# Performance work log

Measured on AMD Instinct MI355X. Metric: run time of the kernel, lower is better.

The kernel has to match this reference:

```python
import jax, jax.numpy as jnp
import numpy as np

N = 50000
E = 1600000
F = 128
G = 64  # number of graphs in the batch


def gat_layer(x, src, dst, W, a_src, a_dst, bias, heads, out_dim, concat):
    n = x.shape[0]
    h = (x @ W).reshape(n, heads, out_dim)                      # [N,H,D]
    alpha_src = jnp.sum(h * a_src, axis=-1)                     # [N,H]
    alpha_dst = jnp.sum(h * a_dst, axis=-1)                     # [N,H]
    e = jax.nn.leaky_relu(alpha_src[src] + alpha_dst[dst], negative_slope=0.2)  # [E,H]
    # segment softmax over edges grouped by destination node
    m = jax.ops.segment_max(e, dst, num_segments=n)
    m = jnp.where(jnp.isfinite(m), m, 0.0)
    ex = jnp.exp(e - m[dst])
    denom = jax.ops.segment_sum(ex, dst, num_segments=n)
    alpha = ex / (denom[dst] + 1e-16)                           # [E,H]
    msg = h[src] * alpha[:, :, None]                            # [E,H,D]
    out = jax.ops.segment_sum(msg, dst, num_segments=n)         # [N,H,D]
    if concat:
        out = out.reshape(n, heads * out_dim)
    else:
        out = out.mean(axis=1)
    return out + bias


def setup_inputs() -> dict:
    key = jax.random.key(0)
    ks = jax.random.split(key, 12)
    x = jax.random.normal(ks[0], (N, F), dtype=jnp.float32)
    edge_index = jax.random.randint(ks[1], (2, E), 0, N, dtype=jnp.int32)
    batch = jnp.sort(jax.random.randint(ks[2], (N,), 0, G, dtype=jnp.int32))
    s = 0.1
    W1 = jax.random.normal(ks[3], (F, 4 * 32), dtype=jnp.float32) * s
    a_src1 = jax.random.normal(ks[4], (4, 32), dtype=jnp.float32) * s
    a_dst1 = jax.random.normal(ks[5], (4, 32), dtype=jnp.float32) * s
    b1 = jnp.zeros((4 * 32,), dtype=jnp.float32)
    W2 = jax.random.normal(ks[6], (4 * 32, 2 * 16), dtype=jnp.float32) * s
    a_src2 = jax.random.normal(ks[7], (2, 16), dtype=jnp.float32) * s
    a_dst2 = jax.random.normal(ks[8], (2, 16), dtype=jnp.float32) * s
    b2 = jnp.zeros((16,), dtype=jnp.float32)
    fcW = jax.random.normal(ks[9], (16, 1), dtype=jnp.float32) * s
    fcb = jnp.zeros((1,), dtype=jnp.float32)
    return {"x": x, "edge_index": edge_index, "batch": batch,
            "W1": W1, "a_src1": a_src1, "a_dst1": a_dst1, "b1": b1,
            "W2": W2, "a_src2": a_src2, "a_dst2": a_dst2, "b2": b2,
            "fcW": fcW, "fcb": fcb}


def reference(x, edge_index, batch, W1, a_src1, a_dst1, b1, W2, a_src2, a_dst2, b2, fcW, fcb):
    n = x.shape[0]
    # PyG GATConv default: add self loops
    loops = jnp.arange(n, dtype=edge_index.dtype)
    src = jnp.concatenate([edge_index[0], loops])
    dst = jnp.concatenate([edge_index[1], loops])
    # eval mode: dropouts are no-ops
    h = jax.nn.relu(gat_layer(x, src, dst, W1, a_src1, a_dst1, b1, 4, 32, True))
    h = gat_layer(h, src, dst, W2, a_src2, a_dst2, b2, 2, 16, False)
    # global mean pool over graphs
    sums = jax.ops.segment_sum(h, batch, num_segments=G)        # [G,16]
    counts = jax.ops.segment_sum(jnp.ones((n,), h.dtype), batch, num_segments=G)
    pooled = sums / jnp.maximum(counts, 1.0)[:, None]
    return pooled @ fcW + fcb                                   # [G,1]
```

## Files before the change

kernel.cpp:

```cpp
#include <hip/hip_runtime.h>

#define LRELU(x) ((x) > 0.f ? (x) : 0.2f*(x))
typedef unsigned int uint;

__device__ inline unsigned short f2bf(float f) {
    union { float f; unsigned u; } v; v.f = f;
    unsigned r = v.u + 0x7FFF + ((v.u >> 16) & 1);
    return (unsigned short)(r >> 16);
}
__device__ inline uint packbf(float a, float b) {
    return (uint)f2bf(a) | ((uint)f2bf(b) << 16);
}
__device__ inline float bflo(uint u){ union{uint u; float f;}v; v.u = u<<16; return v.f; }
__device__ inline float bfhi(uint u){ union{uint u; float f;}v; v.u = u & 0xFFFF0000u; return v.f; }
__device__ inline float f4get(const float4& v, int i) {
    return i==0 ? v.x : i==1 ? v.y : i==2 ? v.z : v.w;
}


#define CSR_SHIFT 7
#define CSR_NBLK  512

__global__ __launch_bounds__(256) void bucket_count_kernel(
    const int* __restrict__ dst, int E, int chunk, int nb,
    int* __restrict__ blockCntT)
{
    __shared__ int cnt[1024];
    int t = threadIdx.x, k = blockIdx.x;
    for (int i = t; i < nb; i += 256) cnt[i] = 0;
    __syncthreads();
    int e0 = k * chunk, e1 = min(e0 + chunk, E);
    for (int e = e0 + t; e < e1; e += 256)
        atomicAdd(&cnt[dst[e] >> CSR_SHIFT], 1);
    __syncthreads();
    for (int b = t; b < nb; b += 256)
        blockCntT[b * CSR_NBLK + k] = cnt[b];
}

__global__ __launch_bounds__(512) void row_scan_kernel(
    int* __restrict__ blockCntT, int* __restrict__ tot)
{
    __shared__ int sm[512];
    int b = blockIdx.x, t = threadIdx.x;
    int* row = blockCntT + b * CSR_NBLK;
    int v = row[t];
    sm[t] = v;
    __syncthreads();
    for (int off = 1; off < 512; off <<= 1) {
        int u = (t >= off) ? sm[t - off] : 0;
        __syncthreads(); sm[t] += u; __syncthreads();
    }
    row[t] = sm[t] - v;
    if (t == 511) tot[b] = sm[511];
}

__global__ __launch_bounds__(1024) void total_scan_kernel(
    const int* __restrict__ tot, int nb, int* __restrict__ bucketBase)
{
    __shared__ int sm[1024];
    int t = threadIdx.x;
    int v = (t < nb) ? tot[t] : 0;
    sm[t] = v;
    __syncthreads();
    for (int off = 1; off < 1024; off <<= 1) {
        int u = (t >= off) ? sm[t - off] : 0;
        __syncthreads(); sm[t] += u; __syncthreads();
    }
    if (t < nb) bucketBase[t] = sm[t] - v;
    if (t == 1023) bucketBase[nb] = sm[1023];
}

__global__ __launch_bounds__(256) void bucket_scatter_kernel(
    const int* __restrict__ src, const int* __restrict__ dst, int E, int chunk, int nb,
    const int* __restrict__ blockCntT, const int* __restrict__ bucketBase,
    uint* __restrict__ ebuf)
{
    __shared__ int cur[1024];
    int t = threadIdx.x, k = blockIdx.x;
    for (int b = t; b < nb; b += 256)
        cur[b] = bucketBase[b] + blockCntT[b * CSR_NBLK + k];
    __syncthreads();
    int e0 = k * chunk, e1 = min(e0 + chunk, E);
    for (int e = e0 + t; e < e1; e += 256) {
        int d = dst[e], s_ = src[e];
        int pos = atomicAdd(&cur[d >> CSR_SHIFT], 1);
        ebuf[pos] = ((uint)s_ << 7) | (uint)(d & 127);
    }
}

__global__ __launch_bounds__(256) void local_csr_kernel(
    const uint* __restrict__ ebuf, const int* __restrict__ bucketBase,
    int n, int E, int* __restrict__ rowptr, int* __restrict__ csr)
{
    __shared__ int lbase[1 << CSR_SHIFT];
    __shared__ int lcur[1 << CSR_SHIFT];
    __shared__ int ldeg[1 << CSR_SHIFT];
    int b = blockIdx.x, t = threadIdx.x;
    int n0 = b << CSR_SHIFT;
    int base = bucketBase[b], end = bucketBase[b + 1];
    if (t < (1 << CSR_SHIFT)) ldeg[t] = 0;
    __syncthreads();
    for (int e = base + t; e < end; e += 256)
        atomicAdd(&ldeg[ebuf[e] & 127], 1);
    __syncthreads();
    if (t == 0) {
        int run = base;
        for (int i = 0; i < (1 << CSR_SHIFT); ++i) {
            lbase[i] = run; lcur[i] = run; run += ldeg[i];
        }
    }
    __syncthreads();
    int node = n0 + t;
    if (t < (1 << CSR_SHIFT) && node < n) rowptr[node] = lbase[t];
    if (b == 0 && t == 0) rowptr[n] = E;
    for (int e = base + t; e < end; e += 256) {
        uint ed = ebuf[e];
        int pos = atomicAdd(&lcur[ed & 127], 1);
        csr[pos] = (int)(ed >> 7);
    }
}


template<int COLS, int HEADS>
__global__ __launch_bounds__(256) void gemm_alpha_kernel(
    const float* __restrict__ x, const float* __restrict__ W,
    const float* __restrict__ a_src, const float* __restrict__ a_dst,
    uint* __restrict__ hq, float* __restrict__ as_out,
    float* __restrict__ ad_out, int n)
{
    constexpr int K = 128;
    constexpr int CPT = COLS / 8;
    constexpr int NPT = 4;
    constexpr int DIM = COLS / HEADS;
    constexpr int TPH = DIM / CPT;
    constexpr int NSLOT = COLS / 4;
    __shared__ float4 WL[K * NSLOT];

    int t = threadIdx.x;
    for (int idx = t * 4; idx < K * COLS; idx += 1024) {
        float4 w = *(const float4*)(W + idx);
        int k = idx / COLS, c = idx % COLS;
        int slot = c >> 2;
        if (COLS == 128) slot = (slot >> 2) | ((slot & 3) << 3);
        WL[k * NSLOT + slot] = w;
    }
    __syncthreads();

    int m_ = t & 7;
    int node0 = blockIdx.x * (32 * NPT) + (t >> 3) * NPT;
    if (node0 >= n) return;
    int c0 = m_ * CPT;

    const float* xr[NPT];
#pragma unroll
    for (int i = 0; i < NPT; i++) xr[i] = x + (size_t)min(node0 + i, n - 1) * K;

    float acc[NPT][CPT];
#pragma unroll
    for (int i = 0; i < NPT; i++)
#pragma unroll
        for (int q = 0; q < CPT; q++) acc[i][q] = 0.f;

    for (int k4 = 0; k4 < K; k4 += 4) {
        float4 xv[NPT];
#pragma unroll
        for (int i = 0; i < NPT; i++) xv[i] = *(const float4*)(xr[i] + k4);
#pragma unroll
        for (int kk = 0; kk < 4; kk++) {
#pragma unroll
            for (int j = 0; j < CPT / 4; j++) {
                int slot = (COLS == 128) ? (m_ | (j << 3)) : m_;
                float4 w = WL[(k4 + kk) * NSLOT + slot];
#pragma unroll
                for (int i = 0; i < NPT; i++) {
                    float xa = f4get(xv[i], kk);
                    acc[i][j*4+0] += xa * w.x;
                    acc[i][j*4+1] += xa * w.y;
                    acc[i][j*4+2] += xa * w.z;
                    acc[i][j*4+3] += xa * w.w;
                }
            }
        }
    }

    int head = c0 / DIM, lc = c0 - head * DIM;
    float asc[CPT], adc[CPT];
#pragma unroll
    for (int q = 0; q < CPT; q++) {
        asc[q] = a_src[head * DIM + lc + q];
        adc[q] = a_dst[head * DIM + lc + q];
    }

#pragma unroll
    for (int i = 0; i < NPT; i++) {
        int node = node0 + i;
        if (node >= n) break;
        if constexpr (COLS == 128) {
            uint wds[4];
#pragma unroll
            for (int j = 0; j < 4; j++) {
                int u = 0;
                u = __builtin_amdgcn_cvt_pk_fp8_f32(acc[i][j*4+0], acc[i][j*4+1], u, false);
                u = __builtin_amdgcn_cvt_pk_fp8_f32(acc[i][j*4+2], acc[i][j*4+3], u, true);
                wds[j] = (uint)u;
            }
            *(uint4*)(hq + (size_t)node * 32 + m_ * 4) = make_uint4(wds[0], wds[1], wds[2], wds[3]);
        } else {
            uint w0 = packbf(acc[i][0], acc[i][1]);
            uint w1 = packbf(acc[i][2], acc[i][3]);
            *(uint2*)(hq + (size_t)node * 16 + m_ * 2) = make_uint2(w0, w1);
        }
        float ps = 0.f, pd = 0.f;
#pragma unroll
        for (int q = 0; q < CPT; q++) {
            ps += acc[i][q] * asc[q];
            pd += acc[i][q] * adc[q];
        }
#pragma unroll
        for (int off = 1; off < TPH; off <<= 1) {
            ps += __shfl_xor(ps, off);
            pd += __shfl_xor(pd, off);
        }
        if ((m_ & (TPH - 1)) == 0) {
            as_out[node * HEADS + head] = ps;
            ad_out[node * HEADS + head] = pd;
        }
    }
}


__global__ __launch_bounds__(256) void agg1_kernel(
    const float* __restrict__ as1f, const float* __restrict__ ad1f,
    const uint* __restrict__ h1q, const int* __restrict__ rowptr,
    const int* __restrict__ csr, const float* __restrict__ b1,
    float* __restrict__ hout, int n)
{
    int t = threadIdx.x;
    int w = t >> 6, tw = t & 63;
    int g = tw >> 3, l = tw & 7;
    int head = l >> 1;
    int node = blockIdx.x * 4 + w;
    if (node >= n) return;

    float adh = ad1f[node * 4 + head];
    int rp = rowptr[node], re = rowptr[node + 1];

    float acc[16];
#pragma unroll
    for (int i = 0; i < 16; i++) acc[i] = 0.f;
    float den = 0.f;

#pragma unroll 2
    for (int e = rp + g; e < re; e += 8) {
        int s = csr[e];
        float a = as1f[s * 4 + head];
        uint4 u = *(const uint4*)(h1q + ((size_t)s << 5) + (l << 2));
        float ex = __expf(LRELU(a + adh));
        den += ex;
        uint ua[4] = {u.x, u.y, u.z, u.w};
#pragma unroll
        for (int j = 0; j < 4; j++) {
            auto p0 = __builtin_amdgcn_cvt_pk_f32_fp8(ua[j], false);
            auto p1 = __builtin_amdgcn_cvt_pk_f32_fp8(ua[j], true);
            acc[j*4+0] += ex * p0[0]; acc[j*4+1] += ex * p0[1];
            acc[j*4+2] += ex * p1[0]; acc[j*4+3] += ex * p1[1];
        }
    }

    if (g == 0) {
        float a = as1f[node * 4 + head];
        float ex = __expf(LRELU(a + adh));
        den += ex;
        uint4 u = *(const uint4*)(h1q + ((size_t)node << 5) + (l << 2));
        uint ua[4] = {u.x, u.y, u.z, u.w};
#pragma unroll
        for (int j = 0; j < 4; j++) {
            auto p0 = __builtin_amdgcn_cvt_pk_f32_fp8(ua[j], false);
            auto p1 = __builtin_amdgcn_cvt_pk_f32_fp8(ua[j], true);
            acc[j*4+0] += ex * p0[0]; acc[j*4+1] += ex * p0[1];
            acc[j*4+2] += ex * p1[0]; acc[j*4+3] += ex * p1[1];
        }
    }

#pragma unroll
    for (int i = 0; i < 16; i++) {
        acc[i] += __shfl_xor(acc[i], 8);
        acc[i] += __shfl_xor(acc[i], 16);
        acc[i] += __shfl_xor(acc[i], 32);
    }
    den += __shfl_xor(den, 8);
    den += __shfl_xor(den, 16);
    den += __shfl_xor(den, 32);

    if (g == 0) {
        float inv = 1.f / (den + 1e-16f);
        const float4* b4 = (const float4*)b1;
#pragma unroll
        for (int j = 0; j < 4; j++) {
            float4 bv = b4[(l << 2) + j];
            float4 o;
            o.x = fmaxf(acc[j*4+0] * inv + bv.x, 0.f);
            o.y = fmaxf(acc[j*4+1] * inv + bv.y, 0.f);
            o.z = fmaxf(acc[j*4+2] * inv + bv.z, 0.f);
            o.w = fmaxf(acc[j*4+3] * inv + bv.w, 0.f);
            ((float4*)hout)[(size_t)node * 32 + (l << 2) + j] = o;
        }
    }
}


__global__ __launch_bounds__(256) void agg2_kernel(
    const float* __restrict__ as2f, const float* __restrict__ ad2f,
    const uint* __restrict__ h2q, const int* __restrict__ rowptr,
    const int* __restrict__ csr, const float* __restrict__ b2,
    float* __restrict__ hf, int n)
{
    int t = threadIdx.x;
    int w = t >> 6, tw = t & 63;
    int g = tw >> 3, l = tw & 7;
    int head = l >> 2;
    int node = blockIdx.x * 4 + w;
    if (node >= n) return;

    float adh = ad2f[node * 2 + head];
    int rp = rowptr[node], re = rowptr[node + 1];

    float acc[4] = {0.f, 0.f, 0.f, 0.f};
    float den = 0.f;

#pragma unroll 2
    for (int e = rp + g; e < re; e += 8) {
        int s = csr[e];
        float a = as2f[s * 2 + head];
        uint2 u = *(const uint2*)(h2q + ((size_t)s << 4) + (l << 1));
        float ex = __expf(LRELU(a + adh));
        den += ex;
        acc[0] += ex * bflo(u.x); acc[1] += ex * bfhi(u.x);
        acc[2] += ex * bflo(u.y); acc[3] += ex * bfhi(u.y);
    }

    if (g == 0) {
        float a = as2f[node * 2 + head];
        float ex = __expf(LRELU(a + adh));
        den += ex;
        uint2 u = *(const uint2*)(h2q + ((size_t)node << 4) + (l << 1));
        acc[0] += ex * bflo(u.x); acc[1] += ex * bfhi(u.x);
        acc[2] += ex * bflo(u.y); acc[3] += ex * bfhi(u.y);
    }

#pragma unroll
    for (int i = 0; i < 4; i++) {
        acc[i] += __shfl_xor(acc[i], 8);
        acc[i] += __shfl_xor(acc[i], 16);
        acc[i] += __shfl_xor(acc[i], 32);
    }
    den += __shfl_xor(den, 8);
    den += __shfl_xor(den, 16);
    den += __shfl_xor(den, 32);

    float inv = 1.f / (den + 1e-16f);
    float v0 = acc[0] * inv, v1 = acc[1] * inv, v2 = acc[2] * inv, v3 = acc[3] * inv;
    float o0 = 0.5f * (v0 + __shfl_xor(v0, 4));
    float o1 = 0.5f * (v1 + __shfl_xor(v1, 4));
    float o2 = 0.5f * (v2 + __shfl_xor(v2, 4));
    float o3 = 0.5f * (v3 + __shfl_xor(v3, 4));
    if (g == 0 && l < 4) {
        float4 o;
        o.x = o0 + b2[4*l+0]; o.y = o1 + b2[4*l+1];
        o.z = o2 + b2[4*l+2]; o.w = o3 + b2[4*l+3];
        *(float4*)(hf + (size_t)node * 16 + 4 * l) = o;
    }
}


__global__ __launch_bounds__(256) void pool_kernel(
    const float* __restrict__ hf, const int* __restrict__ batch,
    float* __restrict__ sums, float* __restrict__ counts, int n)
{
    int t = threadIdx.x;
    int d = t & 15, j = t >> 4;
    int base = blockIdx.x * 256 + j * 16;
    float run = 0.f, cnt = 0.f;
    int cg = -1;
    for (int i = 0; i < 16; ++i) {
        int nn = base + i;
        if (nn >= n) break;
        int g = batch[nn];
        if (g != cg) {
            if (cg >= 0) { atomicAdd(&sums[cg * 16 + d], run); if (d == 0) atomicAdd(&counts[cg], cnt); }
            cg = g; run = 0.f; cnt = 0.f;
        }
        run += hf[(size_t)nn * 16 + d];
        cnt += 1.f;
    }
    if (cg >= 0) { atomicAdd(&sums[cg * 16 + d], run); if (d == 0) atomicAdd(&counts[cg], cnt); }
}

__global__ void final_kernel(const float* __restrict__ sums, const float* __restrict__ counts,
                             const float* __restrict__ fcW, const float* __restrict__ fcb,
                             float* __restrict__ out, int G)
{
    int g = blockIdx.x * 64 + threadIdx.x;
    if (g < G) {
        float c = fmaxf(counts[g], 1.f);
        float s = 0.f;
        for (int dd = 0; dd < 16; ++dd) s += (sums[g * 16 + dd] / c) * fcW[dd];
        out[g] = s + fcb[0];
    }
}


extern "C" void kernel_launch(void* const* d_in, const int* in_sizes, int n_in,
                              void* d_out, int out_size, void* d_ws, size_t ws_size,
                              hipStream_t stream)
{
    const float* x      = (const float*)d_in[0];
    const int*   ei     = (const int*)d_in[1];
    const int*   batch  = (const int*)d_in[2];
    const float* W1     = (const float*)d_in[3];
    const float* a_src1 = (const float*)d_in[4];
    const float* a_dst1 = (const float*)d_in[5];
    const float* b1     = (const float*)d_in[6];
    const float* W2     = (const float*)d_in[7];
    const float* a_src2 = (const float*)d_in[8];
    const float* a_dst2 = (const float*)d_in[9];
    const float* b2     = (const float*)d_in[10];
    const float* fcW    = (const float*)d_in[11];
    const float* fcb    = (const float*)d_in[12];
    float* out = (float*)d_out;

    int n = in_sizes[0] / 128;
    int E = in_sizes[1] / 2;
    int G = out_size;
    const int* srcA = ei;
    const int* dstA = ei + E;

    int nb = (n + (1 << CSR_SHIFT) - 1) >> CSR_SHIFT;
    int chunk = (E + CSR_NBLK - 1) / CSR_NBLK;

    char* p = (char*)d_ws;
    auto alloc = [&](size_t bytes) { char* r = p; p += (bytes + 255) & ~(size_t)255; return r; };
    int*   blockCntT  = (int*)alloc((size_t)nb * CSR_NBLK * 4);
    int*   tot        = (int*)alloc((size_t)nb * 4);
    int*   bucketBase = (int*)alloc((size_t)(nb + 1) * 4);
    int*   rowptr     = (int*)alloc((size_t)(n + 1) * 4);
    int*   csr        = (int*)alloc((size_t)E * 4);
    uint*  h1q        = (uint*)alloc((size_t)n * 32 * 4);
    float* as1        = (float*)alloc((size_t)n * 16);
    float* ad1        = (float*)alloc((size_t)n * 16);
    float* hrelu      = (float*)alloc((size_t)n * 128 * 4);
    uint*  h2q        = (uint*)alloc((size_t)n * 16 * 4);
    float* as2        = (float*)alloc((size_t)n * 8);
    float* ad2        = (float*)alloc((size_t)n * 8);
    float* hf         = (float*)alloc((size_t)n * 16 * 4);
    float* sums       = (float*)alloc((size_t)G * 16 * 4 + (size_t)G * 4);
    float* counts     = sums + G * 16;

    uint* ebuf = (uint*)hrelu;

    hipMemsetAsync(sums, 0, (size_t)G * 16 * 4 + (size_t)G * 4, stream);

    bucket_count_kernel<<<CSR_NBLK, 256, 0, stream>>>(dstA, E, chunk, nb, blockCntT);
    row_scan_kernel<<<nb, 512, 0, stream>>>(blockCntT, tot);
    total_scan_kernel<<<1, 1024, 0, stream>>>(tot, nb, bucketBase);
    bucket_scatter_kernel<<<CSR_NBLK, 256, 0, stream>>>(srcA, dstA, E, chunk, nb,
                                                        blockCntT, bucketBase, ebuf);
    local_csr_kernel<<<nb, 256, 0, stream>>>(ebuf, bucketBase, n, E, rowptr, csr);

    int gb = (n + 127) / 128;
    gemm_alpha_kernel<128, 4><<<gb, 256, 0, stream>>>(x, W1, a_src1, a_dst1, h1q, as1, ad1, n);
    agg1_kernel<<<(n + 3) / 4, 256, 0, stream>>>(as1, ad1, h1q, rowptr, csr, b1, hrelu, n);
    gemm_alpha_kernel<32, 2><<<gb, 256, 0, stream>>>(hrelu, W2, a_src2, a_dst2, h2q, as2, ad2, n);
    agg2_kernel<<<(n + 3) / 4, 256, 0, stream>>>(as2, ad2, h2q, rowptr, csr, b2, hf, n);
    pool_kernel<<<(n + 255) / 256, 256, 0, stream>>>(hf, batch, sums, counts, n);
    final_kernel<<<1, 64, 0, stream>>>(sums, counts, fcW, fcb, out, G);
}
```

Baseline: 195.9 us.

## Precompute per-edge attention exponentials in fp16 before aggregation kernels

Adds a destination array to the CSR build and two per-edge kernels that compute exp(leaky_relu(alpha_src+alpha_dst)) for all heads once, storing them as packed fp16 in CSR order. The aggregation kernels then read these values with a coalesced load instead of doing a random gather of alpha_src plus an exp per lane, and their inner-loop unroll grows from 2 to 4. This costs extra kernel launches, an extra E-sized dst array write, and per-edge exp buffers (8 bytes per edge for layer 1). Storing the exponentials in fp16 reduces precision and can overflow for large logits.

Result: slower. 244.3 us (+24.8%).

```diff
diff --git a/kernel.cpp b/kernel.cpp
--- a/kernel.cpp
+++ b/kernel.cpp
@@ -2,11 +2,12 @@
 
 #define LRELU(x) ((x) > 0.f ? (x) : 0.2f*(x))
 typedef unsigned int uint;
-
-__device__ inline unsigned short f2bf(float f) {
+typedef unsigned short ushort;
+
+__device__ inline ushort f2bf(float f) {
     union { float f; unsigned u; } v; v.f = f;
     unsigned r = v.u + 0x7FFF + ((v.u >> 16) & 1);
-    return (unsigned short)(r >> 16);
+    return (ushort)(r >> 16);
 }
 __device__ inline uint packbf(float a, float b) {
     return (uint)f2bf(a) | ((uint)f2bf(b) << 16);
@@ -16,6 +17,8 @@
 __device__ inline float f4get(const float4& v, int i) {
     return i==0 ? v.x : i==1 ? v.y : i==2 ? v.z : v.w;
 }
+__device__ inline ushort f2h(float f){ _Float16 h=(_Float16)f; union{_Float16 h; ushort u;}v; v.h=h; return v.u; }
+__device__ inline float h2f(ushort u){ union{ushort u; _Float16 h;}v; v.u=u; return (float)v.h; }
 
 
 #define CSR_SHIFT 7
@@ -90,7 +93,8 @@
 
 __global__ __launch_bounds__(256) void local_csr_kernel(
     const uint* __restrict__ ebuf, const int* __restrict__ bucketBase,
-    int n, int E, int* __restrict__ rowptr, int* __restrict__ csr)
+    int n, int E, int* __restrict__ rowptr, int* __restrict__ csr,
+    int* __restrict__ dstarr)
 {
     __shared__ int lbase[1 << CSR_SHIFT];
     __shared__ int lcur[1 << CSR_SHIFT];
@@ -115,9 +119,42 @@
     if (b == 0 && t == 0) rowptr[n] = E;
     for (int e = base + t; e < end; e += 256) {
         uint ed = ebuf[e];
-        int pos = atomicAdd(&lcur[ed & 127], 1);
+        int ld = (int)(ed & 127);
+        int pos = atomicAdd(&lcur[ld], 1);
         csr[pos] = (int)(ed >> 7);
-    }
+        dstarr[pos] = n0 + ld;
+    }
+}
+
+
+__global__ __launch_bounds__(256) void edge_ex1_kernel(
+    const float4* __restrict__ as1, const float4* __restrict__ ad1,
+    const int* __restrict__ csr, const int* __restrict__ dstarr,
+    ushort* __restrict__ exq, int E)
+{
+    int p = blockIdx.x * 256 + threadIdx.x;
+    if (p >= E) return;
+    int s = csr[p], d = dstarr[p];
+    float4 a = as1[s], b = ad1[d];
+    ushort4 o;
+    o.x = f2h(__expf(LRELU(a.x + b.x)));
+    o.y = f2h(__expf(LRELU(a.y + b.y)));
+    o.z = f2h(__expf(LRELU(a.z + b.z)));
+    o.w = f2h(__expf(LRELU(a.w + b.w)));
+    *(ushort4*)(exq + (size_t)p * 4) = o;
+}
+
+__global__ __launch_bounds__(256) void edge_ex2_kernel(
+    const float2* __restrict__ as2, const float2* __restrict__ ad2,
+    const int* __restrict__ csr, const int* __restrict__ dstarr,
+    uint* __restrict__ exq, int E)
+{
+    int p = blockIdx.x * 256 + threadIdx.x;
+    if (p >= E) return;
+    int s = csr[p], d = dstarr[p];
+    float2 a = as2[s], b = ad2[d];
+    exq[p] = (uint)f2h(__expf(LRELU(a.x + b.x)))
+           | ((uint)f2h(__expf(LRELU(a.y + b.y))) << 16);
 }
 
 
@@ -231,9 +268,9 @@
 
 __global__ __launch_bounds__(256) void agg1_kernel(
     const float* __restrict__ as1f, const float* __restrict__ ad1f,
-    const uint* __restrict__ h1q, const int* __restrict__ rowptr,
-    const int* __restrict__ csr, const float* __restrict__ b1,
-    float* __restrict__ hout, int n)
+    const ushort* __restrict__ exq, const uint* __restrict__ h1q,
+    const int* __restrict__ rowptr, const int* __restrict__ csr,
+    const float* __restrict__ b1, float* __restrict__ hout, int n)
 {
     int t = threadIdx.x;
     int w = t >> 6, tw = t & 63;
@@ -242,7 +279,6 @@
     int node = blockIdx.x * 4 + w;
     if (node >= n) return;
 
-    float adh = ad1f[node * 4 + head];
     int rp = rowptr[node], re = rowptr[node + 1];
 
     float acc[16];
@@ -250,12 +286,13 @@
     for (int i = 0; i < 16; i++) acc[i] = 0.f;
     float den = 0.f;
 
-#pragma unroll 2
+#pragma unroll 4
     for (int e = rp + g; e < re; e += 8) {
         int s = csr[e];
-        float a = as1f[s * 4 + head];
+        uint2 q = *(const uint2*)(exq + (size_t)e * 4);
+        uint hw = (head & 2) ? q.y : q.x;
+        float ex = h2f((ushort)((head & 1) ? (hw >> 16) : (hw & 0xFFFF)));
         uint4 u = *(const uint4*)(h1q + ((size_t)s << 5) + (l << 2));
-        float ex = __expf(LRELU(a + adh));
         den += ex;
         uint ua[4] = {u.x, u.y, u.z, u.w};
 #pragma unroll
@@ -269,6 +306,7 @@
 
     if (g == 0) {
         float a = as1f[node * 4 + head];
+        float adh = ad1f[node * 4 + head];
         float ex = __expf(LRELU(a + adh));
         den += ex;
         uint4 u = *(const uint4*)(h1q + ((size_t)node << 5) + (l << 2));
@@ -311,9 +349,9 @@
 
 __global__ __launch_bounds__(256) void agg2_kernel(
     const float* __restrict__ as2f, const float* __restrict__ ad2f,
-    const uint* __restrict__ h2q, const int* __restrict__ rowptr,
-    const int* __restrict__ csr, const float* __restrict__ b2,
-    float* __restrict__ hf, int n)
+    const uint* __restrict__ exq, const uint* __restrict__ h2q,
+    const int* __restrict__ rowptr, const int* __restrict__ csr,
+    const float* __restrict__ b2, float* __restrict__ hf, int n)
 {
     int t = threadIdx.x;
     int w = t >> 6, tw = t & 63;
@@ -322,18 +360,17 @@
     int node = blockIdx.x * 4 + w;
     if (node >= n) return;
 
-    float adh = ad2f[node * 2 + head];
     int rp = rowptr[node], re = rowptr[node + 1];
 
     float acc[4] = {0.f, 0.f, 0.f, 0.f};
     float den = 0.f;
 
-#pragma unroll 2
+#pragma unroll 4
     for (int e = rp + g; e < re; e += 8) {
         int s = csr[e];
-        float a = as2f[s * 2 + head];
+        uint q = exq[e];
+        float ex = h2f((ushort)(head ? (q >> 16) : (q & 0xFFFF)));
         uint2 u = *(const uint2*)(h2q + ((size_t)s << 4) + (l << 1));
-        float ex = __expf(LRELU(a + adh));
         den += ex;
         acc[0] += ex * bflo(u.x); acc[1] += ex * bfhi(u.x);
         acc[2] += ex * bflo(u.y); acc[3] += ex * bfhi(u.y);
@@ -341,6 +378,7 @@
 
     if (g == 0) {
         float a = as2f[node * 2 + head];
+        float adh = ad2f[node * 2 + head];
         float ex = __expf(LRELU(a + adh));
         den += ex;
         uint2 u = *(const uint2*)(h2q + ((size_t)node << 4) + (l << 1));
@@ -445,7 +483,11 @@
     int*   bucketBase = (int*)alloc((size_t)(nb + 1) * 4);
     int*   rowptr     = (int*)alloc((size_t)(n + 1) * 4);
     int*   csr        = (int*)alloc((size_t)E * 4);
-    uint*  h1q        = (uint*)alloc((size_t)n * 32 * 4);
+    int*   dstarr     = (int*)alloc((size_t)E * 4);
+    size_t h1bytes = (size_t)n * 32 * 4;
+    size_t ex2bytes = (size_t)E * 4;
+    uint*  h1q        = (uint*)alloc(h1bytes > ex2bytes ? h1bytes : ex2bytes);
+    ushort* exq1      = (ushort*)alloc((size_t)E * 8);
     float* as1        = (float*)alloc((size_t)n * 16);
     float* ad1        = (float*)alloc((size_t)n * 16);
     float* hrelu      = (float*)alloc((size_t)n * 128 * 4);
@@ -457,6 +499,7 @@
     float* counts     = sums + G * 16;
 
     uint* ebuf = (uint*)hrelu;
+    uint* exq2 = (uint*)h1q;
 
     hipMemsetAsync(sums, 0, (size_t)G * 16 * 4 + (size_t)G * 4, stream);
 
@@ -465,13 +508,18 @@
     total_scan_kernel<<<1, 1024, 0, stream>>>(tot, nb, bucketBase);
     bucket_scatter_kernel<<<CSR_NBLK, 256, 0, stream>>>(srcA, dstA, E, chunk, nb,
                                                         blockCntT, bucketBase, ebuf);
-    local_csr_kernel<<<nb, 256, 0, stream>>>(ebuf, bucketBase, n, E, rowptr, csr);
+    local_csr_kernel<<<nb, 256, 0, stream>>>(ebuf, bucketBase, n, E, rowptr, csr, dstarr);
 
     int gb = (n + 127) / 128;
+    int eb = (E + 255) / 256;
     gemm_alpha_kernel<128, 4><<<gb, 256, 0, stream>>>(x, W1, a_src1, a_dst1, h1q, as1, ad1, n);
-    agg1_kernel<<<(n + 3) / 4, 256, 0, stream>>>(as1, ad1, h1q, rowptr, csr, b1, hrelu, n);
+    edge_ex1_kernel<<<eb, 256, 0, stream>>>((const float4*)as1, (const float4*)ad1,
+                                            csr, dstarr, exq1, E);
+    agg1_kernel<<<(n + 3) / 4, 256, 0, stream>>>(as1, ad1, exq1, h1q, rowptr, csr, b1, hrelu, n);
     gemm_alpha_kernel<32, 2><<<gb, 256, 0, stream>>>(hrelu, W2, a_src2, a_dst2, h2q, as2, ad2, n);
-    agg2_kernel<<<(n + 3) / 4, 256, 0, stream>>>(as2, ad2, h2q, rowptr, csr, b2, hf, n);
+    edge_ex2_kernel<<<eb, 256, 0, stream>>>((const float2*)as2, (const float2*)ad2,
+                                            csr, dstarr, exq2, E);
+    agg2_kernel<<<(n + 3) / 4, 256, 0, stream>>>(as2, ad2, exq2, h2q, rowptr, csr, b2, hf, n);
     pool_kernel<<<(n + 255) / 256, 256, 0, stream>>>(hf, batch, sums, counts, n);
     final_kernel<<<1, 64, 0, stream>>>(sums, counts, fcW, fcb, out, G);
 }
```
